# Optimization experiments

Hardware: AMD Instinct MI355X
Metric: run time of the kernel (lower is better)

The kernel has to match this reference:

```python
import math
import jax, jax.numpy as jnp
import numpy as np

B, S, D, H, HD, FF = 2, 2048, 2048, 16, 128, 5632
EPS = 1e-5


def rmsnorm(h, w):
    # LLaMA RMSNorm: x * rsqrt(mean(x^2) + eps) * weight
    return h * jax.lax.rsqrt(jnp.mean(h * h, axis=-1, keepdims=True) + EPS) * w


def cross_attn(q_in, kv_in, wq, wk, wv, wo):
    # start_pos = 0 and zero-init cache => keys/values are exactly the fresh xk/xv
    b, sq, _ = q_in.shape
    sk = kv_in.shape[1]
    q = (q_in @ wq.T).reshape(b, sq, H, HD)
    k = (kv_in @ wk.T).reshape(b, sk, H, HD)
    v = (kv_in @ wv.T).reshape(b, sk, H, HD)
    scores = jnp.einsum('bqhd,bkhd->bhqk', q, k) / math.sqrt(HD)
    p = jax.nn.softmax(scores.astype(jnp.float32), axis=-1).astype(q.dtype)
    o = jnp.einsum('bhqk,bkhd->bqhd', p, v).reshape(b, sq, H * HD)
    return o @ wo.T


def llama_output(h, residual_in, w1, w2, w3, norm_w):
    # SwiGLU FFN then post-residual RMSNorm (as in LLaMAOutput)
    ff = (jax.nn.silu(h @ w1.T) * (h @ w3.T)) @ w2.T
    return rmsnorm(ff + residual_in, norm_w)


def setup_inputs() -> dict:
    key = jax.random.key(0)
    ks = jax.random.split(key, 20)
    w = lambda k, shape: jax.random.normal(k, shape, jnp.float32) * 0.02
    return {
        'x': jax.random.normal(ks[0], (B, S, D), jnp.float32),
        'y': jax.random.normal(ks[1], (B, S, D), jnp.float32),
        'attn_norm_w': jnp.ones((D,), jnp.float32),
        'wq_x': w(ks[2], (D, D)), 'wk_x': w(ks[3], (D, D)),
        'wv_x': w(ks[4], (D, D)), 'wo_x': w(ks[5], (D, D)),
        'wq_y': w(ks[6], (D, D)), 'wk_y': w(ks[7], (D, D)),
        'wv_y': w(ks[8], (D, D)), 'wo_y': w(ks[9], (D, D)),
        'w1_x': w(ks[10], (FF, D)), 'w2_x': w(ks[11], (D, FF)), 'w3_x': w(ks[12], (FF, D)),
        'ffn_norm_x': jnp.ones((D,), jnp.float32),
        'w1_y': w(ks[13], (FF, D)), 'w2_y': w(ks[14], (D, FF)), 'w3_y': w(ks[15], (FF, D)),
        'ffn_norm_y': jnp.ones((D,), jnp.float32),
        'start_pos': 0,
    }


def reference(x, y, attn_norm_w,
              wq_x, wk_x, wv_x, wo_x,
              wq_y, wk_y, wv_y, wo_y,
              w1_x, w2_x, w3_x, ffn_norm_x,
              w1_y, w2_y, w3_y, ffn_norm_y,
              start_pos):
    del start_pos  # 0: cache slice [:, :0+S] equals fresh xk/xv
    xn = rmsnorm(x, attn_norm_w)
    yn = rmsnorm(y, attn_norm_w)
    out_x = cross_attn(xn, yn, wq_x, wk_x, wv_x, wo_x)
    out_y = cross_attn(yn, xn, wq_y, wk_y, wv_y, wo_y)
    return (llama_output(out_x, x, w1_x, w2_x, w3_x, ffn_norm_x),
            llama_output(out_y, y, w1_y, w2_y, w3_y, ffn_norm_y))
```

## Files before the change

kernel.cpp:

```cpp
#include <hip/hip_runtime.h>
#include <cstdio>
#include <cstdint>
#include <cstddef>

#define B_ 2
#define S_ 2048
#define D_ 2048
#define H_ 16
#define HD_ 128
#define FF_ 5632

typedef unsigned short u16;
typedef float f32x4 __attribute__((ext_vector_type(4)));
typedef __bf16 bf16x8 __attribute__((ext_vector_type(8)));
typedef short s16x8 __attribute__((ext_vector_type(8)));
typedef short s16x4 __attribute__((ext_vector_type(4)));

__device__ __forceinline__ u16 f2bf(float f) {
  unsigned u = __builtin_bit_cast(unsigned, f);
  u += 0x7fffu + ((u >> 16) & 1u);
  return (u16)(u >> 16);
}
__device__ __forceinline__ float bf2f(u16 h) {
  unsigned u = ((unsigned)h) << 16;
  return __builtin_bit_cast(float, u);
}

__device__ __forceinline__ void async_ld16(const void* g, void* l) {
  __builtin_amdgcn_global_load_lds(
      (__attribute__((address_space(1))) void*)(unsigned long long)g,
      (__attribute__((address_space(3))) void*)(unsigned)(unsigned long long)l,
      16, 0, 0);
}

__global__ __launch_bounds__(256) void k_cvt_bf16(
    const float* __restrict__ in, u16* __restrict__ out, int n8) {
  const int i = blockIdx.x * 256 + threadIdx.x;
  if (i >= n8) return;
  const float4* p = (const float4*)in + (size_t)i * 2;
  const float4 a = p[0], b = p[1];
  s16x8 o;
  o[0] = (short)f2bf(a.x); o[1] = (short)f2bf(a.y);
  o[2] = (short)f2bf(a.z); o[3] = (short)f2bf(a.w);
  o[4] = (short)f2bf(b.x); o[5] = (short)f2bf(b.y);
  o[6] = (short)f2bf(b.z); o[7] = (short)f2bf(b.w);
  *(s16x8*)(out + (size_t)i * 8) = o;
}

__global__ __launch_bounds__(256) void k_rmsnorm_bf16(
    const float* __restrict__ x, const float* __restrict__ w, u16* __restrict__ out) {
  const int row = blockIdx.x;
  const int t = threadIdx.x;
  const float* xr = x + (size_t)row * D_;
  const float4 a = ((const float4*)xr)[t];
  const float4 b = ((const float4*)xr)[t + 256];
  float ss = a.x * a.x + a.y * a.y + a.z * a.z + a.w * a.w +
             b.x * b.x + b.y * b.y + b.z * b.z + b.w * b.w;
#pragma unroll
  for (int off = 1; off < 64; off <<= 1) ss += __shfl_xor(ss, off);
  __shared__ float red[4];
  if ((t & 63) == 0) red[t >> 6] = ss;
  __syncthreads();
  const float scale =
      rsqrtf((red[0] + red[1] + red[2] + red[3]) * (1.0f / (float)D_) + 1e-5f);
  const float4 wa = ((const float4*)w)[t];
  const float4 wb = ((const float4*)w)[t + 256];
  u16* orow = out + (size_t)row * D_;
  s16x4 o0, o1;
  o0[0] = (short)f2bf(a.x * scale * wa.x);
  o0[1] = (short)f2bf(a.y * scale * wa.y);
  o0[2] = (short)f2bf(a.z * scale * wa.z);
  o0[3] = (short)f2bf(a.w * scale * wa.w);
  o1[0] = (short)f2bf(b.x * scale * wb.x);
  o1[1] = (short)f2bf(b.y * scale * wb.y);
  o1[2] = (short)f2bf(b.z * scale * wb.z);
  o1[3] = (short)f2bf(b.w * scale * wb.w);
  *(s16x4*)(orow + t * 4) = o0;
  *(s16x4*)(orow + (t + 256) * 4) = o1;
}

__global__ __launch_bounds__(256) void k_add_rmsnorm(
    const float* __restrict__ ff, const float* __restrict__ res,
    const float* __restrict__ w, float* __restrict__ out) {
  const int row = blockIdx.x;
  const int t = threadIdx.x;
  const float4 fa = ((const float4*)(ff + (size_t)row * D_))[t];
  const float4 fb = ((const float4*)(ff + (size_t)row * D_))[t + 256];
  const float4 ra = ((const float4*)(res + (size_t)row * D_))[t];
  const float4 rb = ((const float4*)(res + (size_t)row * D_))[t + 256];
  float4 ha, hb2;
  ha.x = fa.x + ra.x; ha.y = fa.y + ra.y; ha.z = fa.z + ra.z; ha.w = fa.w + ra.w;
  hb2.x = fb.x + rb.x; hb2.y = fb.y + rb.y; hb2.z = fb.z + rb.z; hb2.w = fb.w + rb.w;
  float ss = ha.x * ha.x + ha.y * ha.y + ha.z * ha.z + ha.w * ha.w +
             hb2.x * hb2.x + hb2.y * hb2.y + hb2.z * hb2.z + hb2.w * hb2.w;
#pragma unroll
  for (int off = 1; off < 64; off <<= 1) ss += __shfl_xor(ss, off);
  __shared__ float red[4];
  if ((t & 63) == 0) red[t >> 6] = ss;
  __syncthreads();
  const float scale =
      rsqrtf((red[0] + red[1] + red[2] + red[3]) * (1.0f / (float)D_) + 1e-5f);
  const float4 wa = ((const float4*)w)[t];
  const float4 wb = ((const float4*)w)[t + 256];
  float4 o0, o1;
  o0.x = ha.x * scale * wa.x; o0.y = ha.y * scale * wa.y;
  o0.z = ha.z * scale * wa.z; o0.w = ha.w * scale * wa.w;
  o1.x = hb2.x * scale * wb.x; o1.y = hb2.y * scale * wb.y;
  o1.z = hb2.z * scale * wb.z; o1.w = hb2.w * scale * wb.w;
  float* orow = out + (size_t)row * D_;
  ((float4*)orow)[t] = o0;
  ((float4*)orow)[t + 256] = o1;
}

__global__ __launch_bounds__(256) void k_silu_mul(
    const u16* __restrict__ g, const u16* __restrict__ u, u16* __restrict__ out) {
  const size_t i = ((size_t)blockIdx.x * 256 + threadIdx.x) * 8;
  s16x8 gv = *(const s16x8*)(g + i);
  s16x8 uv = *(const s16x8*)(u + i);
  s16x8 ov;
#pragma unroll
  for (int j = 0; j < 8; j++) {
    float gf = bf2f((u16)gv[j]);
    float uf = bf2f((u16)uv[j]);
    float s = gf / (1.0f + __expf(-gf));
    ov[j] = (short)f2bf(s * uf);
  }
  *(s16x8*)(out + i) = ov;
}

template <int OUTF32>
__global__ __launch_bounds__(256, 2) void k_gemm_bt(
    const u16* __restrict__ A, const u16* __restrict__ Bm, void* __restrict__ Cp,
    int M, int N, int K) {
  __shared__ __align__(16) u16 sA[128 * 32];
  __shared__ __align__(16) u16 sB[128 * 32];
  const int tid = threadIdx.x;
  const int lane = tid & 63;
  const int wave = tid >> 6;
  const int l15 = lane & 15;
  const int quad = lane >> 4;
  const int wm = (wave >> 1) * 64;
  const int wn = (wave & 1) * 64;
  const int bm = blockIdx.y * 128;
  const int bn = blockIdx.x * 128;

  const int sr = tid >> 2;
  const int sc = (tid & 3) * 8;
  const u16* pa = A + (size_t)(bm + sr) * K + sc;
  const u16* pb = Bm + (size_t)(bn + sr) * K + sc;
  u16* la = &sA[tid * 8];
  u16* lb = &sB[tid * 8];
  const size_t half = (size_t)64 * K;

  f32x4 acc[4][4] = {};
  const u16* ra = &sA[(wm + l15) * 32 + quad * 8];
  const u16* rb = &sB[(wn + l15) * 32 + quad * 8];

  for (int k0 = 0; k0 < K; k0 += 32) {
    async_ld16(pa, la);
    async_ld16(pa + half, la + 2048);
    async_ld16(pb, lb);
    async_ld16(pb + half, lb + 2048);
    pa += 32;
    pb += 32;
    __syncthreads();
    bf16x8 af[4], bfr[4];
#pragma unroll
    for (int i = 0; i < 4; i++) af[i] = *(const bf16x8*)(ra + i * 512);
#pragma unroll
    for (int j = 0; j < 4; j++) bfr[j] = *(const bf16x8*)(rb + j * 512);
#pragma unroll
    for (int i = 0; i < 4; i++)
#pragma unroll
      for (int j = 0; j < 4; j++)
        acc[i][j] = __builtin_amdgcn_mfma_f32_16x16x32_bf16(af[i], bfr[j],
                                                            acc[i][j], 0, 0, 0);
    __syncthreads();
  }

#pragma unroll
  for (int i = 0; i < 4; i++)
#pragma unroll
    for (int j = 0; j < 4; j++) {
      const int row0 = bm + wm + i * 16 + quad * 4;
      const int col = bn + wn + j * 16 + l15;
      if (OUTF32) {
        float* C = (float*)Cp;
#pragma unroll
        for (int r = 0; r < 4; r++)
          C[(size_t)(row0 + r) * N + col] = acc[i][j][r];
      } else {
        u16* C = (u16*)Cp;
#pragma unroll
        for (int r = 0; r < 4; r++)
          C[(size_t)(row0 + r) * N + col] = f2bf(acc[i][j][r]);
      }
    }
}

__global__ __launch_bounds__(256) void k_flash(
    const u16* __restrict__ Qm, const u16* __restrict__ Km,
    const u16* __restrict__ Vm, u16* __restrict__ Om) {
  __shared__ __align__(16) u16 sK[32 * 136];
  __shared__ __align__(16) u16 sVT[128 * 40];
  __shared__ __align__(16) u16 sP[4][32 * 40];

  const int tid = threadIdx.x;
  const int lane = tid & 63;
  const int wave = tid >> 6;
  const int l15 = lane & 15;
  const int quad = lane >> 4;

  const int b = blockIdx.z;
  const int h = blockIdx.y;
  const int q0 = blockIdx.x * 128;

  const size_t headoff = ((size_t)b * S_) * (size_t)D_ + (size_t)h * HD_;

  bf16x8 aq[2][4];
#pragma unroll
  for (int mi = 0; mi < 2; mi++) {
    const u16* qp = Qm + headoff + (size_t)(q0 + wave * 32 + mi * 16 + l15) * D_;
#pragma unroll
    for (int c = 0; c < 4; c++)
      aq[mi][c] = *(const bf16x8*)(qp + c * 32 + quad * 8);
  }

  f32x4 o[2][8] = {};
  float l[2][4] = {};

  const int skr = tid >> 3;
  const int skc = (tid & 7) * 16;
  const int vkr = tid & 31;
  const int vc0 = (tid >> 5) * 16;

  const float rs = 0.08838834764831845f;

  for (int k0 = 0; k0 < S_; k0 += 32) {
    __syncthreads();
    {
      const u16* kp = Km + headoff + (size_t)(k0 + skr) * D_ + skc;
      s16x8 kv0 = *(const s16x8*)(kp);
      s16x8 kv1 = *(const s16x8*)(kp + 8);
      *(s16x8*)(&sK[skr * 136 + skc]) = kv0;
      *(s16x8*)(&sK[skr * 136 + skc + 8]) = kv1;
      const u16* vp = Vm + headoff + (size_t)(k0 + vkr) * D_ + vc0;
      s16x8 vv0 = *(const s16x8*)(vp);
      s16x8 vv1 = *(const s16x8*)(vp + 8);
#pragma unroll
      for (int j = 0; j < 8; j++) sVT[(vc0 + j) * 40 + vkr] = (u16)vv0[j];
#pragma unroll
      for (int j = 0; j < 8; j++) sVT[(vc0 + 8 + j) * 40 + vkr] = (u16)vv1[j];
    }
    __syncthreads();

    bf16x8 bk[2][4];
#pragma unroll
    for (int nt = 0; nt < 2; nt++)
#pragma unroll
      for (int c = 0; c < 4; c++)
        bk[nt][c] = *(const bf16x8*)(&sK[(nt * 16 + l15) * 136 + c * 32 + quad * 8]);

#pragma unroll
    for (int mi = 0; mi < 2; mi++) {
      f32x4 s[2] = {};
#pragma unroll
      for (int nt = 0; nt < 2; nt++)
#pragma unroll
        for (int c = 0; c < 4; c++)
          s[nt] = __builtin_amdgcn_mfma_f32_16x16x32_bf16(aq[mi][c], bk[nt][c],
                                                          s[nt], 0, 0, 0);
#pragma unroll
      for (int nt = 0; nt < 2; nt++)
#pragma unroll
        for (int r = 0; r < 4; r++) {
          float pv = __expf(s[nt][r] * rs);
          l[mi][r] += pv;
          sP[wave][(mi * 16 + quad * 4 + r) * 40 + nt * 16 + l15] = f2bf(pv);
        }
    }

    bf16x8 ap[2];
#pragma unroll
    for (int mi = 0; mi < 2; mi++)
      ap[mi] = *(const bf16x8*)(&sP[wave][(mi * 16 + l15) * 40 + quad * 8]);
#pragma unroll
    for (int ht = 0; ht < 8; ht++) {
      bf16x8 bv = *(const bf16x8*)(&sVT[(ht * 16 + l15) * 40 + quad * 8]);
#pragma unroll
      for (int mi = 0; mi < 2; mi++)
        o[mi][ht] = __builtin_amdgcn_mfma_f32_16x16x32_bf16(ap[mi], bv,
                                                            o[mi][ht], 0, 0, 0);
    }
  }

#pragma unroll
  for (int mi = 0; mi < 2; mi++)
#pragma unroll
    for (int r = 0; r < 4; r++) {
      float s = l[mi][r];
      s += __shfl_xor(s, 1);
      s += __shfl_xor(s, 2);
      s += __shfl_xor(s, 4);
      s += __shfl_xor(s, 8);
      l[mi][r] = 1.0f / s;
    }
#pragma unroll
  for (int mi = 0; mi < 2; mi++)
#pragma unroll
    for (int r = 0; r < 4; r++) {
      const size_t ro =
          headoff + (size_t)(q0 + wave * 32 + mi * 16 + quad * 4 + r) * D_;
      const float inv = l[mi][r];
#pragma unroll
      for (int ht = 0; ht < 8; ht++)
        Om[ro + ht * 16 + l15] = f2bf(o[mi][ht][r] * inv);
    }
}

extern "C" void kernel_launch(void* const* d_in, const int* in_sizes, int n_in,
                              void* d_out, int out_size, void* d_ws, size_t ws_size,
                              hipStream_t stream) {
  (void)in_sizes; (void)n_in; (void)out_size;

  const float* x = (const float*)d_in[0];
  const float* y = (const float*)d_in[1];
  const float* attn_norm_w = (const float*)d_in[2];
  const float* wq[2] = {(const float*)d_in[3], (const float*)d_in[7]};
  const float* wk[2] = {(const float*)d_in[4], (const float*)d_in[8]};
  const float* wv[2] = {(const float*)d_in[5], (const float*)d_in[9]};
  const float* wo[2] = {(const float*)d_in[6], (const float*)d_in[10]};
  const float* w1[2] = {(const float*)d_in[11], (const float*)d_in[15]};
  const float* w2[2] = {(const float*)d_in[12], (const float*)d_in[16]};
  const float* w3[2] = {(const float*)d_in[13], (const float*)d_in[17]};
  const float* fnw[2] = {(const float*)d_in[14], (const float*)d_in[18]};

  char* ws = (char*)d_ws;
  const size_t ACT = (size_t)4096 * 2048 * 2;
  const size_t WSLOT = (size_t)FF_ * D_ * 2;
  const size_t GBUF = (size_t)4096 * FF_ * 2;
  u16* xn = (u16*)(ws);
  u16* yn = (u16*)(ws + ACT);
  u16* qb = (u16*)(ws + 2 * ACT);
  u16* kb = (u16*)(ws + 3 * ACT);
  u16* vb = (u16*)(ws + 4 * ACT);
  u16* ao = (u16*)(ws + 5 * ACT);
  u16* hb = (u16*)(ws + 6 * ACT);
  u16* wslot = (u16*)(ws + 7 * ACT);
  u16* g = (u16*)(ws + 7 * ACT + WSLOT);
  u16* uu = (u16*)(ws + 7 * ACT + WSLOT + GBUF);
  float* ff = (float*)(ws + 7 * ACT + WSLOT + 2 * GBUF);
  const size_t NEED = 7 * ACT + WSLOT + 2 * GBUF + (size_t)4096 * 2048 * 4;
  if (ws_size < NEED) {
    fprintf(stderr, "kernel_launch: ws too small: %zu < %zu\n", ws_size, NEED);
    return;
  }

  const float* resid[2] = {x, y};
  float* outp[2] = {(float*)d_out, (float*)d_out + (size_t)8388608};

  k_rmsnorm_bf16<<<4096, 256, 0, stream>>>(x, attn_norm_w, xn);
  k_rmsnorm_bf16<<<4096, 256, 0, stream>>>(y, attn_norm_w, yn);

  const dim3 gproj(16, 32);
  const dim3 gff(44, 32);
  const u16* qin[2] = {xn, yn};
  const u16* kvin[2] = {yn, xn};

  for (int s = 0; s < 2; s++) {
    k_cvt_bf16<<<2048, 256, 0, stream>>>(wq[s], wslot, 524288);
    k_gemm_bt<0><<<gproj, 256, 0, stream>>>(qin[s], wslot, qb, 4096, 2048, 2048);
    k_cvt_bf16<<<2048, 256, 0, stream>>>(wk[s], wslot, 524288);
    k_gemm_bt<0><<<gproj, 256, 0, stream>>>(kvin[s], wslot, kb, 4096, 2048, 2048);
    k_cvt_bf16<<<2048, 256, 0, stream>>>(wv[s], wslot, 524288);
    k_gemm_bt<0><<<gproj, 256, 0, stream>>>(kvin[s], wslot, vb, 4096, 2048, 2048);

    k_flash<<<dim3(16, 16, 2), 256, 0, stream>>>(qb, kb, vb, ao);

    k_cvt_bf16<<<2048, 256, 0, stream>>>(wo[s], wslot, 524288);
    k_gemm_bt<0><<<gproj, 256, 0, stream>>>(ao, wslot, hb, 4096, 2048, 2048);

    k_cvt_bf16<<<5632, 256, 0, stream>>>(w1[s], wslot, 1441792);
    k_gemm_bt<0><<<gff, 256, 0, stream>>>(hb, wslot, g, 4096, 5632, 2048);
    k_cvt_bf16<<<5632, 256, 0, stream>>>(w3[s], wslot, 1441792);
    k_gemm_bt<0><<<gff, 256, 0, stream>>>(hb, wslot, uu, 4096, 5632, 2048);
    k_silu_mul<<<11264, 256, 0, stream>>>(g, uu, g);
    k_cvt_bf16<<<5632, 256, 0, stream>>>(w2[s], wslot, 1441792);
    k_gemm_bt<1><<<gproj, 256, 0, stream>>>(g, wslot, ff, 4096, 2048, 5632);

    k_add_rmsnorm<<<4096, 256, 0, stream>>>(ff, resid[s], fnw[s], outp[s]);
  }
}
```

Measured before the change: 1.881 ms.

## Fuse QKV and W1/W3 GEMMs, emit transposed V from GEMM epilogue

Concatenates weights so each input's projections run as a single GEMM: Q for its own stream plus K and V for the other stream (N=6144), and W1 with W3 (N=11264). The QKV GEMM epilogue writes V already transposed, so the flash kernel loads V^T with vector loads and no longer scatters a transpose into shared memory. The aim is fewer kernel launches, larger grids that fill the GPU better, and cheaper V staging. In exchange, workspace buffers are aliased more aggressively, SiLU indexing is strided, and the transposed V stores from the epilogue are only 8 bytes wide.

```diff
diff --git a/kernel.cpp b/kernel.cpp
--- a/kernel.cpp
+++ b/kernel.cpp
@@ -113,10 +113,12 @@
 }
 
 __global__ __launch_bounds__(256) void k_silu_mul(
-    const u16* __restrict__ g, const u16* __restrict__ u, u16* __restrict__ out) {
-  const size_t i = ((size_t)blockIdx.x * 256 + threadIdx.x) * 8;
-  s16x8 gv = *(const s16x8*)(g + i);
-  s16x8 uv = *(const s16x8*)(u + i);
+    const u16* __restrict__ gcat, u16* __restrict__ out) {
+  const int idx = blockIdx.x * 256 + threadIdx.x;
+  const int row = idx / 704;
+  const int c = (idx - row * 704) * 8;
+  const s16x8 gv = *(const s16x8*)(gcat + (size_t)row * 11264 + c);
+  const s16x8 uv = *(const s16x8*)(gcat + (size_t)row * 11264 + 5632 + c);
   s16x8 ov;
 #pragma unroll
   for (int j = 0; j < 8; j++) {
@@ -125,13 +127,13 @@
     float s = gf / (1.0f + __expf(-gf));
     ov[j] = (short)f2bf(s * uf);
   }
-  *(s16x8*)(out + i) = ov;
-}
-
-template <int OUTF32>
+  *(s16x8*)(out + (size_t)row * 5632 + c) = ov;
+}
+
+template <int MODE>
 __global__ __launch_bounds__(256, 2) void k_gemm_bt(
     const u16* __restrict__ A, const u16* __restrict__ Bm, void* __restrict__ Cp,
-    int M, int N, int K) {
+    u16* __restrict__ VT, int M, int N, int K, int ldc) {
   __shared__ __align__(16) u16 sA[128 * 32];
   __shared__ __align__(16) u16 sB[128 * 32];
   const int tid = threadIdx.x;
@@ -178,29 +180,43 @@
     __syncthreads();
   }
 
+  if (MODE == 2 && bn >= 4096) {
+#pragma unroll
+    for (int i = 0; i < 4; i++)
+#pragma unroll
+      for (int j = 0; j < 4; j++) {
+        const int row0 = bm + wm + i * 16 + quad * 4;
+        const int cv = bn + wn + j * 16 + l15 - 4096;
+        s16x4 o;
+#pragma unroll
+        for (int r = 0; r < 4; r++) o[r] = (short)f2bf(acc[i][j][r]);
+        *(s16x4*)(VT + (size_t)cv * 4096 + row0) = o;
+      }
+    return;
+  }
 #pragma unroll
   for (int i = 0; i < 4; i++)
 #pragma unroll
     for (int j = 0; j < 4; j++) {
       const int row0 = bm + wm + i * 16 + quad * 4;
       const int col = bn + wn + j * 16 + l15;
-      if (OUTF32) {
+      if (MODE == 1) {
         float* C = (float*)Cp;
 #pragma unroll
         for (int r = 0; r < 4; r++)
-          C[(size_t)(row0 + r) * N + col] = acc[i][j][r];
+          C[(size_t)(row0 + r) * ldc + col] = acc[i][j][r];
       } else {
         u16* C = (u16*)Cp;
 #pragma unroll
         for (int r = 0; r < 4; r++)
-          C[(size_t)(row0 + r) * N + col] = f2bf(acc[i][j][r]);
+          C[(size_t)(row0 + r) * ldc + col] = f2bf(acc[i][j][r]);
       }
     }
 }
 
 __global__ __launch_bounds__(256) void k_flash(
     const u16* __restrict__ Qm, const u16* __restrict__ Km,
-    const u16* __restrict__ Vm, u16* __restrict__ Om) {
+    const u16* __restrict__ VTm, u16* __restrict__ Om) {
   __shared__ __align__(16) u16 sK[32 * 136];
   __shared__ __align__(16) u16 sVT[128 * 40];
   __shared__ __align__(16) u16 sP[4][32 * 40];
@@ -214,13 +230,13 @@
   const int b = blockIdx.z;
   const int h = blockIdx.y;
   const int q0 = blockIdx.x * 128;
-
-  const size_t headoff = ((size_t)b * S_) * (size_t)D_ + (size_t)h * HD_;
+  const int LDQ = 6144;
+  const size_t rowbase = (size_t)b * 2048;
 
   bf16x8 aq[2][4];
 #pragma unroll
   for (int mi = 0; mi < 2; mi++) {
-    const u16* qp = Qm + headoff + (size_t)(q0 + wave * 32 + mi * 16 + l15) * D_;
+    const u16* qp = Qm + (rowbase + q0 + wave * 32 + mi * 16 + l15) * LDQ + h * 128;
 #pragma unroll
     for (int c = 0; c < 4; c++)
       aq[mi][c] = *(const bf16x8*)(qp + c * 32 + quad * 8);
@@ -229,28 +245,27 @@
   f32x4 o[2][8] = {};
   float l[2][4] = {};
 
-  const int skr = tid >> 3;
-  const int skc = (tid & 7) * 16;
-  const int vkr = tid & 31;
-  const int vc0 = (tid >> 5) * 16;
+  const int kr0 = tid >> 4;
+  const int kc = (tid & 15) * 8;
+  const int vhd = tid >> 2;
+  const int vko = (tid & 3) * 8;
+
+  const u16* Kbase = Km + rowbase * LDQ + h * 128;
+  const u16* Vbase = VTm + (size_t)(h * 128) * 4096 + rowbase;
 
   const float rs = 0.08838834764831845f;
 
   for (int k0 = 0; k0 < S_; k0 += 32) {
     __syncthreads();
     {
-      const u16* kp = Km + headoff + (size_t)(k0 + skr) * D_ + skc;
-      s16x8 kv0 = *(const s16x8*)(kp);
-      s16x8 kv1 = *(const s16x8*)(kp + 8);
-      *(s16x8*)(&sK[skr * 136 + skc]) = kv0;
-      *(s16x8*)(&sK[skr * 136 + skc + 8]) = kv1;
-      const u16* vp = Vm + headoff + (size_t)(k0 + vkr) * D_ + vc0;
-      s16x8 vv0 = *(const s16x8*)(vp);
-      s16x8 vv1 = *(const s16x8*)(vp + 8);
-#pragma unroll
-      for (int j = 0; j < 8; j++) sVT[(vc0 + j) * 40 + vkr] = (u16)vv0[j];
-#pragma unroll
-      for (int j = 0; j < 8; j++) sVT[(vc0 + 8 + j) * 40 + vkr] = (u16)vv1[j];
+      const s16x8 kv0 = *(const s16x8*)(Kbase + (size_t)(k0 + kr0) * LDQ + kc);
+      const s16x8 kv1 = *(const s16x8*)(Kbase + (size_t)(k0 + kr0 + 16) * LDQ + kc);
+      const s16x8 vv0 = *(const s16x8*)(Vbase + (size_t)vhd * 4096 + k0 + vko);
+      const s16x8 vv1 = *(const s16x8*)(Vbase + (size_t)(vhd + 64) * 4096 + k0 + vko);
+      *(s16x8*)(&sK[kr0 * 136 + kc]) = kv0;
+      *(s16x8*)(&sK[(kr0 + 16) * 136 + kc]) = kv1;
+      *(s16x8*)(&sVT[vhd * 40 + vko]) = vv0;
+      *(s16x8*)(&sVT[(vhd + 64) * 40 + vko]) = vv1;
     }
     __syncthreads();
 
@@ -310,7 +325,8 @@
 #pragma unroll
     for (int r = 0; r < 4; r++) {
       const size_t ro =
-          headoff + (size_t)(q0 + wave * 32 + mi * 16 + quad * 4 + r) * D_;
+          (rowbase + q0 + wave * 32 + mi * 16 + quad * 4 + r) * (size_t)D_ +
+          (size_t)h * HD_;
       const float inv = l[mi][r];
 #pragma unroll
       for (int ht = 0; ht < 8; ht++)
@@ -336,58 +352,71 @@
   const float* fnw[2] = {(const float*)d_in[14], (const float*)d_in[18]};
 
   char* ws = (char*)d_ws;
-  const size_t ACT = (size_t)4096 * 2048 * 2;
-  const size_t WSLOT = (size_t)FF_ * D_ * 2;
-  const size_t GBUF = (size_t)4096 * FF_ * 2;
-  u16* xn = (u16*)(ws);
-  u16* yn = (u16*)(ws + ACT);
-  u16* qb = (u16*)(ws + 2 * ACT);
-  u16* kb = (u16*)(ws + 3 * ACT);
-  u16* vb = (u16*)(ws + 4 * ACT);
-  u16* ao = (u16*)(ws + 5 * ACT);
-  u16* hb = (u16*)(ws + 6 * ACT);
-  u16* wslot = (u16*)(ws + 7 * ACT);
-  u16* g = (u16*)(ws + 7 * ACT + WSLOT);
-  u16* uu = (u16*)(ws + 7 * ACT + WSLOT + GBUF);
-  float* ff = (float*)(ws + 7 * ACT + WSLOT + 2 * GBUF);
-  const size_t NEED = 7 * ACT + WSLOT + 2 * GBUF + (size_t)4096 * 2048 * 4;
+  const size_t A0 = 0;
+  const size_t A1 = 16777216;
+  const size_t W_ = 33554432;
+  const size_t Q1 = 79691776;
+  const size_t Q2 = 130023424;
+  const size_t V1 = 180355072;
+  const size_t V2 = 197132288;
+  const size_t GB = 213909504;
+  const size_t NEED = 260046848;
   if (ws_size < NEED) {
     fprintf(stderr, "kernel_launch: ws too small: %zu < %zu\n", ws_size, NEED);
     return;
   }
+  u16* xn = (u16*)(ws + A0);
+  u16* yn = (u16*)(ws + A1);
+  u16* wslot = (u16*)(ws + W_);
+  u16* qkvA = (u16*)(ws + Q1);
+  u16* qkvB = (u16*)(ws + Q2);
+  u16* vtA = (u16*)(ws + V1);
+  u16* vtB = (u16*)(ws + V2);
+  u16* ao = (u16*)(ws + A0);
+  u16* hbx = (u16*)(ws + A1);
+  u16* hby = (u16*)(ws + V1);
+  u16* gcat = (u16*)(ws + Q1);
+  u16* gbuf = (u16*)(ws + GB);
+  float* ff = (float*)(ws + Q1);
+
+  const size_t WOFF = (size_t)2048 * 2048;
+
+  k_rmsnorm_bf16<<<4096, 256, 0, stream>>>(x, attn_norm_w, xn);
+  k_rmsnorm_bf16<<<4096, 256, 0, stream>>>(y, attn_norm_w, yn);
+
+  const dim3 gqkv(48, 32);
+  const dim3 gproj(16, 32);
+  const dim3 gw13(88, 32);
+
+  k_cvt_bf16<<<2048, 256, 0, stream>>>(wq[0], wslot, 524288);
+  k_cvt_bf16<<<2048, 256, 0, stream>>>(wk[1], wslot + WOFF, 524288);
+  k_cvt_bf16<<<2048, 256, 0, stream>>>(wv[1], wslot + 2 * WOFF, 524288);
+  k_gemm_bt<2><<<gqkv, 256, 0, stream>>>(xn, wslot, qkvA, vtA, 4096, 6144, 2048, 6144);
+  k_cvt_bf16<<<2048, 256, 0, stream>>>(wq[1], wslot, 524288);
+  k_cvt_bf16<<<2048, 256, 0, stream>>>(wk[0], wslot + WOFF, 524288);
+  k_cvt_bf16<<<2048, 256, 0, stream>>>(wv[0], wslot + 2 * WOFF, 524288);
+  k_gemm_bt<2><<<gqkv, 256, 0, stream>>>(yn, wslot, qkvB, vtB, 4096, 6144, 2048, 6144);
+
+  k_flash<<<dim3(16, 16, 2), 256, 0, stream>>>(qkvA, qkvB + 2048, vtB, ao);
+  k_cvt_bf16<<<2048, 256, 0, stream>>>(wo[0], wslot, 524288);
+  k_gemm_bt<0><<<gproj, 256, 0, stream>>>(ao, wslot, hbx, nullptr, 4096, 2048, 2048, 2048);
+
+  k_flash<<<dim3(16, 16, 2), 256, 0, stream>>>(qkvB, qkvA + 2048, vtA, ao);
+  k_cvt_bf16<<<2048, 256, 0, stream>>>(wo[1], wslot, 524288);
+  k_gemm_bt<0><<<gproj, 256, 0, stream>>>(ao, wslot, hby, nullptr, 4096, 2048, 2048, 2048);
 
   const float* resid[2] = {x, y};
   float* outp[2] = {(float*)d_out, (float*)d_out + (size_t)8388608};
-
-  k_rmsnorm_bf16<<<4096, 256, 0, stream>>>(x, attn_norm_w, xn);
-  k_rmsnorm_bf16<<<4096, 256, 0, stream>>>(y, attn_norm_w, yn);
-
-  const dim3 gproj(16, 32);
-  const dim3 gff(44, 32);
-  const u16* qin[2] = {xn, yn};
-  const u16* kvin[2] = {yn, xn};
+  u16* hb[2] = {hbx, hby};
+  const size_t W13OFF = (size_t)FF_ * 2048;
 
   for (int s = 0; s < 2; s++) {
-    k_cvt_bf16<<<2048, 256, 0, stream>>>(wq[s], wslot, 524288);
-    k_gemm_bt<0><<<gproj, 256, 0, stream>>>(qin[s], wslot, qb, 4096, 2048, 2048);
-    k_cvt_bf16<<<2048, 256, 0, stream>>>(wk[s], wslot, 524288);
-    k_gemm_bt<0><<<gproj, 256, 0, stream>>>(kvin[s], wslot, kb, 4096, 2048, 2048);
-    k_cvt_bf16<<<2048, 256, 0, stream>>>(wv[s], wslot, 524288);
-    k_gemm_bt<0><<<gproj, 256, 0, stream>>>(kvin[s], wslot, vb, 4096, 2048, 2048);
-
-    k_flash<<<dim3(16, 16, 2), 256, 0, stream>>>(qb, kb, vb, ao);
-
-    k_cvt_bf16<<<2048, 256, 0, stream>>>(wo[s], wslot, 524288);
-    k_gemm_bt<0><<<gproj, 256, 0, stream>>>(ao, wslot, hb, 4096, 2048, 2048);
-
     k_cvt_bf16<<<5632, 256, 0, stream>>>(w1[s], wslot, 1441792);
-    k_gemm_bt<0><<<gff, 256, 0, stream>>>(hb, wslot, g, 4096, 5632, 2048);
-    k_cvt_bf16<<<5632, 256, 0, stream>>>(w3[s], wslot, 1441792);
-    k_gemm_bt<0><<<gff, 256, 0, stream>>>(hb, wslot, uu, 4096, 5632, 2048);
-    k_silu_mul<<<11264, 256, 0, stream>>>(g, uu, g);
+    k_cvt_bf16<<<5632, 256, 0, stream>>>(w3[s], wslot + W13OFF, 1441792);
+    k_gemm_bt<0><<<gw13, 256, 0, stream>>>(hb[s], wslot, gcat, nullptr, 4096, 11264, 2048, 11264);
+    k_silu_mul<<<11264, 256, 0, stream>>>(gcat, gbuf);
     k_cvt_bf16<<<5632, 256, 0, stream>>>(w2[s], wslot, 1441792);
-    k_gemm_bt<1><<<gproj, 256, 0, stream>>>(g, wslot, ff, 4096, 2048, 5632);
-
+    k_gemm_bt<1><<<gproj, 256, 0, stream>>>(gbuf, wslot, ff, nullptr, 4096, 2048, 5632, 2048);
     k_add_rmsnorm<<<4096, 256, 0, stream>>>(ff, resid[s], fnw[s], outp[s]);
   }
 }
```

Result: faster. 1.816 ms (-3.5%).
